# Kernel optimization log

Measured on AMD Instinct MI355X. Metric: run time of the kernel, lower is better.

Reference implementation:

```python
import jax, jax.numpy as jnp
import numpy as np

STRIDES = (8, 16, 32, 64, 128)
SCORE_THR = 0.05
IOU_THR = 0.6
MAX_NUM = 150
USE_CTR = True
B, NC = 64, 20
HW = (128, 64, 32, 16, 8)


def _reshape(feat):
    # [B,C,H,W] -> [B,H*W,C]
    b, c, h, w = feat.shape
    return feat.transpose(0, 2, 3, 1).reshape(b, h * w, c)


def _decode(feat, stride):
    # feat: [B,4,H,W] reg offsets; returns [B,HW,4] boxes (x1,y1,x2,y2)
    _, _, h, w = feat.shape
    xs = jnp.arange(w, dtype=jnp.float32) * stride + (stride // 2)
    ys = jnp.arange(h, dtype=jnp.float32) * stride + (stride // 2)
    yy, xx = jnp.meshgrid(ys, xs, indexing='ij')
    coords = jnp.stack([xx.reshape(-1), yy.reshape(-1)], axis=-1)  # [HW,2]
    off = _reshape(feat) * stride  # [B,HW,4]
    xy1 = coords[None] - off[..., :2]
    xy2 = coords[None] + off[..., 2:]
    return jnp.concatenate([xy1, xy2], axis=-1)


def _nms_single(scores, ids, boxes, valid):
    # scores already sorted descending (from top_k); class-aware offset NMS.
    coord_max = jnp.max(jnp.where(valid[:, None], boxes, -jnp.inf))
    coord_max = jnp.where(jnp.isfinite(coord_max), coord_max, 0.0)
    ob = boxes + (ids.astype(boxes.dtype) * (coord_max + 1.0))[:, None]
    x1, y1, x2, y2 = ob[:, 0], ob[:, 1], ob[:, 2], ob[:, 3]
    areas = (x2 - x1 + 1.0) * (y2 - y1 + 1.0)
    xmin = jnp.maximum(x1[:, None], x1[None, :])
    ymin = jnp.maximum(y1[:, None], y1[None, :])
    xmax = jnp.minimum(x2[:, None], x2[None, :])
    ymax = jnp.minimum(y2[:, None], y2[None, :])
    ow = jnp.clip(xmax - xmin, 0.0)
    oh = jnp.clip(ymax - ymin, 0.0)
    overlap = ow * oh
    union = jnp.clip(areas[:, None] + areas[None, :] - overlap, 1e-10)
    iou = overlap / union  # [N,N]
    n = scores.shape[0]
    idx = jnp.arange(n)

    def body(i, keep):
        sup = keep[i] & (iou[i] > IOU_THR) & (idx > i)
        return keep & ~sup

    return jax.lax.fori_loop(0, n, body, valid)


def setup_inputs() -> dict:
    key = jax.random.key(0)
    ks = jax.random.split(key, 15)
    out = {}
    for li, hw in enumerate(HW):
        out[f'cls{li}'] = jax.random.normal(ks[li], (B, NC, hw, hw), jnp.float32)
        out[f'reg{li}'] = jax.random.uniform(ks[5 + li], (B, 4, hw, hw), jnp.float32)
        out[f'ctr{li}'] = jax.random.normal(ks[10 + li], (B, 1, hw, hw), jnp.float32)
    return out


def reference(cls0, cls1, cls2, cls3, cls4,
              reg0, reg1, reg2, reg3, reg4,
              ctr0, ctr1, ctr2, ctr3, ctr4):
    cls_feats = (cls0, cls1, cls2, cls3, cls4)
    reg_feats = (reg0, reg1, reg2, reg3, reg4)
    ctr_feats = (ctr0, ctr1, ctr2, ctr3, ctr4)

    cls_logits = jnp.concatenate([_reshape(f) for f in cls_feats], axis=1)  # [B,A,NC]
    ctr_logits = jnp.concatenate([_reshape(f) for f in ctr_feats], axis=1)  # [B,A,1]
    cls_preds = jax.nn.sigmoid(cls_logits)
    ctr_preds = jax.nn.sigmoid(ctr_logits)

    cls_scores = jnp.max(cls_preds, axis=-1)  # [B,A]
    cls_ids = jnp.argmax(cls_preds, axis=-1) + 1  # [B,A]
    if USE_CTR:
        cls_scores = jnp.sqrt(cls_scores * ctr_preds[..., 0])

    boxes = jnp.concatenate(
        [_decode(f, s) for f, s in zip(reg_feats, STRIDES)], axis=1)  # [B,A,4]

    top_scores, top_idx = jax.lax.top_k(cls_scores, MAX_NUM)  # sorted desc
    top_ids = jnp.take_along_axis(cls_ids, top_idx, axis=1)
    top_boxes = jnp.take_along_axis(boxes, top_idx[..., None], axis=1)

    valid = top_scores > SCORE_THR
    keep = jax.vmap(_nms_single)(top_scores, top_ids, top_boxes, valid)

    out_scores = jnp.where(keep, top_scores, 0.0)
    out_ids = jnp.where(keep, top_ids, 0)
    out_boxes = jnp.where(keep[..., None], top_boxes, 0.0)
    return out_scores, out_ids, out_boxes, keep
```

## Files before the change

### kernel.cpp

```cpp
#include <hip/hip_runtime.h>
#include <cstdint>
#include <cstddef>

#define NPTS 21824
#define NB   64
#define NCLS 20
#define MAXN 150
#define NCHUNK 11
#define CHSZ 2048
#define CAP  186

typedef unsigned long long u64;
typedef unsigned int u32;


__device__ __forceinline__ u64 bisect_threshold(const u64 (&key)[8], int total,
                                                int (*wcnt)[4], int cap)
{
    const int tid  = threadIdx.x;
    const int lane = tid & 63, wv = tid >> 6;
    u64 T = 0;
    int count = total;
    int it = 0;
    for (int bbit = 62; bbit >= 0; --bbit) {
        if (bbit == 31) bbit = 14;
        if (count <= cap) break;
        u64 Tt = T | (1ull << bbit);
        int c = 0;
        #pragma unroll
        for (int i = 0; i < 8; ++i) c += (key[i] >= Tt) ? 1 : 0;
        for (int off = 32; off; off >>= 1) c += __shfl_xor(c, off);
        if (lane == 0) wcnt[it & 1][wv] = c;
        __syncthreads();
        int tot = wcnt[it & 1][0] + wcnt[it & 1][1]
                + wcnt[it & 1][2] + wcnt[it & 1][3];
        if (tot >= MAXN) { T = Tt; count = tot; }
        ++it;
    }
    return T;
}

__global__ __launch_bounds__(256) void k_part(
    const float* __restrict__ c0, const float* __restrict__ c1,
    const float* __restrict__ c2, const float* __restrict__ c3,
    const float* __restrict__ c4,
    const float* __restrict__ t0, const float* __restrict__ t1,
    const float* __restrict__ t2, const float* __restrict__ t3,
    const float* __restrict__ t4,
    u64* __restrict__ cand)
{
    __shared__ int wcnt[2][4];
    __shared__ int cnt;
    const int tid   = threadIdx.x;
    const int chunk = blockIdx.x;
    const int b     = blockIdx.y;
    const int pl    = tid * 8;
    const int p0    = chunk * CHSZ + pl;

    u64 key[8];
    #pragma unroll
    for (int i = 0; i < 8; ++i) key[i] = 0;

    if (p0 < NPTS) {
        const float* cp; const float* tp; int base; size_t hw;
        if (p0 < 16384)      { cp = c0; tp = t0; base = 0;     hw = 16384; }
        else if (p0 < 20480) { cp = c1; tp = t1; base = 16384; hw = 4096;  }
        else if (p0 < 21504) { cp = c2; tp = t2; base = 20480; hw = 1024;  }
        else if (p0 < 21760) { cp = c3; tp = t3; base = 21504; hw = 256;   }
        else                 { cp = c4; tp = t4; base = 21760; hw = 64;    }
        int q = p0 - base;
        const float* cb = cp + (size_t)b * NCLS * hw + q;

        float4 m0 = *reinterpret_cast<const float4*>(cb);
        float4 m1 = *reinterpret_cast<const float4*>(cb + 4);
        for (int c = 1; c < NCLS; ++c) {
            float4 v0 = *reinterpret_cast<const float4*>(cb + (size_t)c * hw);
            float4 v1 = *reinterpret_cast<const float4*>(cb + (size_t)c * hw + 4);
            m0.x = fmaxf(m0.x, v0.x); m0.y = fmaxf(m0.y, v0.y);
            m0.z = fmaxf(m0.z, v0.z); m0.w = fmaxf(m0.w, v0.w);
            m1.x = fmaxf(m1.x, v1.x); m1.y = fmaxf(m1.y, v1.y);
            m1.z = fmaxf(m1.z, v1.z); m1.w = fmaxf(m1.w, v1.w);
        }
        const float* tb = tp + (size_t)b * hw + q;
        float4 q0 = *reinterpret_cast<const float4*>(tb);
        float4 q1 = *reinterpret_cast<const float4*>(tb + 4);

        float mm[8] = {m0.x, m0.y, m0.z, m0.w, m1.x, m1.y, m1.z, m1.w};
        float cc[8] = {q0.x, q0.y, q0.z, q0.w, q1.x, q1.y, q1.z, q1.w};
        #pragma unroll
        for (int i = 0; i < 8; ++i) {
            float best = 1.0f / (1.0f + expf(-mm[i]));
            float sct  = 1.0f / (1.0f + expf(-cc[i]));
            float sc   = sqrtf(__fmul_rn(best, sct));
            key[i] = ((u64)__float_as_uint(sc) << 32)
                   | (u32)(21823 - (p0 + i));
        }
    }

    u64 T = bisect_threshold(key, CHSZ, wcnt, CAP);

    if (tid == 0) cnt = 0;
    __syncthreads();
    u64* outp = cand + ((size_t)b * NCHUNK + chunk) * CAP;
    #pragma unroll
    for (int i = 0; i < 8; ++i) {
        if (key[i] >= T) {
            int pos = atomicAdd(&cnt, 1);
            if (pos < CAP) outp[pos] = key[i];
        }
    }
    __syncthreads();
    for (int i = cnt + tid; i < CAP; i += 256) outp[i] = 0;
}

__global__ __launch_bounds__(256) void k_sel(
    const u64* __restrict__ cand, u64* __restrict__ srt_g)
{
    const int NC2 = NCHUNK * CAP;
    __shared__ int wcnt[2][4];
    __shared__ int cnt;
    __shared__ u64 win[CAP];

    const int b = blockIdx.x, tid = threadIdx.x;

    u64 key[8];
    #pragma unroll
    for (int j = 0; j < 8; ++j) {
        int i = j * 256 + tid;
        key[j] = (i < NC2) ? cand[(size_t)b * NC2 + i] : 0ull;
    }

    u64 T = bisect_threshold(key, CHSZ, wcnt, CAP);

    if (tid == 0) cnt = 0;
    __syncthreads();
    #pragma unroll
    for (int j = 0; j < 8; ++j) {
        if (key[j] >= T) {
            int pos = atomicAdd(&cnt, 1);
            if (pos < CAP) win[pos] = key[j];
        }
    }
    __syncthreads();
    int C = min(cnt, CAP);
    if (tid < C) {
        u64 mk = win[tid]; int r = 0;
        for (int j = 0; j < C; ++j) r += (win[j] > mk) ? 1 : 0;
        if (r < MAXN) srt_g[(size_t)b * MAXN + r] = mk;
    }
}

__global__ __launch_bounds__(1024) void k_out(
    const float* __restrict__ c0, const float* __restrict__ c1,
    const float* __restrict__ c2, const float* __restrict__ c3,
    const float* __restrict__ c4,
    const float* __restrict__ r0, const float* __restrict__ r1,
    const float* __restrict__ r2, const float* __restrict__ r3,
    const float* __restrict__ r4,
    const u64* __restrict__ srt_g,
    float* __restrict__ out)
{
    __shared__ int   parr[MAXN];
    __shared__ u64   pid[MAXN][4];
    __shared__ float bx0[MAXN], bx1[MAXN], bx2[MAXN], bx3[MAXN];
    __shared__ float ox1[MAXN], oy1[MAXN], ox2[MAXN], oy2[MAXN], area[MAXN];
    __shared__ float sc[MAXN];
    __shared__ int   idv[MAXN];
    __shared__ u64 sup[MAXN][3];
    __shared__ u64 keepw[3];
    __shared__ float shcmax;
    __shared__ float wmax[16];

    const int b = blockIdx.x, tid = threadIdx.x;

    if (tid < MAXN) {
        u64 kk = srt_g[(size_t)b * MAXN + tid];
        sc[tid]   = __uint_as_float((u32)(kk >> 32));
        parr[tid] = 21823 - (int)(kk & 0x7FFFu);
    }
    __syncthreads();

    if (tid < MAXN * 4) {
        int w = tid >> 2, g = tid & 3;
        int p = parr[w];
        const float* cp; int base; size_t hw;
        if (p < 16384)      { cp = c0; base = 0;     hw = 16384; }
        else if (p < 20480) { cp = c1; base = 16384; hw = 4096;  }
        else if (p < 21504) { cp = c2; base = 20480; hw = 1024;  }
        else if (p < 21760) { cp = c3; base = 21504; hw = 256;   }
        else                { cp = c4; base = 21760; hw = 64;    }
        const float* cb = cp + (size_t)b * NCLS * hw + (p - base);
        float best = -1.0f; int bi = 0;
        #pragma unroll
        for (int j = 0; j < 5; ++j) {
            int c = g * 5 + j;
            float v  = cb[(size_t)c * hw];
            float sg = 1.0f / (1.0f + expf(-v));
            if (sg > best) { best = sg; bi = c; }
        }
        pid[w][g] = ((u64)__float_as_uint(best) << 32) | (u32)(31 - bi);
    } else if (tid < MAXN * 4 + MAXN) {
        int w = tid - MAXN * 4;
        int p = parr[w];
        const float* rp; int base, dim, lg, st;
        if (p < 16384)      { rp = r0; base = 0;     dim = 128; lg = 7; st = 8;   }
        else if (p < 20480) { rp = r1; base = 16384; dim = 64;  lg = 6; st = 16;  }
        else if (p < 21504) { rp = r2; base = 20480; dim = 32;  lg = 5; st = 32;  }
        else if (p < 21760) { rp = r3; base = 21504; dim = 16;  lg = 4; st = 64;  }
        else                { rp = r4; base = 21760; dim = 8;   lg = 3; st = 128; }
        int q = p - base;
        int y = q >> lg;
        int x = q & (dim - 1);
        float s  = (float)st;
        float cx = (float)(x * st + (st >> 1));
        float cy = (float)(y * st + (st >> 1));
        size_t hw = (size_t)dim * dim;
        const float* rg = rp + (size_t)b * 4 * hw + q;
        float a0 = rg[0], a1 = rg[hw], a2 = rg[2 * hw], a3 = rg[3 * hw];
        bx0[w] = __fsub_rn(cx, __fmul_rn(a0, s));
        bx1[w] = __fsub_rn(cy, __fmul_rn(a1, s));
        bx2[w] = __fadd_rn(cx, __fmul_rn(a2, s));
        bx3[w] = __fadd_rn(cy, __fmul_rn(a3, s));
    }
    __syncthreads();

    if (tid < MAXN) {
        u64 m0 = pid[tid][0], m1 = pid[tid][1];
        u64 m2 = pid[tid][2], m3 = pid[tid][3];
        u64 mbest = m0;
        if (m1 > mbest) mbest = m1;
        if (m2 > mbest) mbest = m2;
        if (m3 > mbest) mbest = m3;
        idv[tid] = (31 - (int)(mbest & 31u)) + 1;
    }
    __syncthreads();

    float m = -INFINITY;
    if (tid < MAXN && sc[tid] > 0.05f)
        m = fmaxf(fmaxf(bx0[tid], bx1[tid]), fmaxf(bx2[tid], bx3[tid]));
    #pragma unroll
    for (int off = 32; off >= 1; off >>= 1) m = fmaxf(m, __shfl_xor(m, off));
    if ((tid & 63) == 0) wmax[tid >> 6] = m;
    if (tid < 192) {
        bool val = (tid < MAXN) && (sc[tid] > 0.05f);
        u64 mask = __ballot(val);
        if ((tid & 63) == 0) keepw[tid >> 6] = mask;
    }
    __syncthreads();
    if (tid == 0) {
        float mm = -INFINITY;
        #pragma unroll
        for (int w = 0; w < 16; ++w) mm = fmaxf(mm, wmax[w]);
        shcmax = isfinite(mm) ? mm : 0.0f;
    }
    __syncthreads();

    float cm1 = __fadd_rn(shcmax, 1.0f);
    if (tid < MAXN) {
        float off = __fmul_rn((float)idv[tid], cm1);
        float X1 = __fadd_rn(bx0[tid], off);
        float Y1 = __fadd_rn(bx1[tid], off);
        float X2 = __fadd_rn(bx2[tid], off);
        float Y2 = __fadd_rn(bx3[tid], off);
        ox1[tid] = X1; oy1[tid] = Y1; ox2[tid] = X2; oy2[tid] = Y2;
        area[tid] = __fmul_rn(__fadd_rn(__fsub_rn(X2, X1), 1.0f),
                              __fadd_rn(__fsub_rn(Y2, Y1), 1.0f));
    }
    __syncthreads();

    if (tid < MAXN * 3) {
        int i = tid / 3;
        int w = tid - i * 3;
        float x1i = ox1[i], y1i = oy1[i], x2i = ox2[i], y2i = oy2[i], ai = area[i];
        u64 bits = 0ull;
        for (int e = 0; e < 64; ++e) {
            int j = w * 64 + e;
            if (j >= MAXN) break;
            float xmin = fmaxf(x1i, ox1[j]);
            float ymin = fmaxf(y1i, oy1[j]);
            float xmax = fminf(x2i, ox2[j]);
            float ymax = fminf(y2i, oy2[j]);
            float ow = fmaxf(__fsub_rn(xmax, xmin), 0.0f);
            float oh = fmaxf(__fsub_rn(ymax, ymin), 0.0f);
            float ov = __fmul_rn(ow, oh);
            float un = fmaxf(__fsub_rn(__fadd_rn(ai, area[j]), ov), 1e-10f);
            float iou = __fdiv_rn(ov, un);
            if (iou > 0.6f) bits |= (1ull << e);
        }
        sup[i][w] = bits;
    }
    __syncthreads();

    if (tid < 64) {
        const int l = tid;
        u64 kw   = (l < 3) ? keepw[l]  : 0ull;
        u64 scur = (l < 3) ? sup[0][l] : 0ull;
        for (int i = 0; i < MAXN; ++i) {
            u64 snext = (l < 3 && i + 1 < MAXN) ? sup[i + 1][l] : 0ull;
            u64 kwwi = __shfl(kw, i >> 6);
            if ((kwwi >> (i & 63)) & 1ull) {
                int lo = l * 64;
                u64 allow;
                if (i < lo)            allow = ~0ull;
                else if (i - lo >= 63) allow = 0ull;
                else                   allow = ~((1ull << (i - lo + 1)) - 1ull);
                kw &= ~(scur & allow);
            }
            scur = snext;
        }
        if (l < 3) keepw[l] = kw;
    }
    __syncthreads();

    if (tid < MAXN) {
        bool kp = (keepw[tid >> 6] >> (tid & 63)) & 1ull;
        int o = b * MAXN + tid;
        float* oSc = out;
        float* oId = out + NB * MAXN;
        float* oBx = out + 2 * NB * MAXN;
        float* oKp = out + 2 * NB * MAXN + NB * MAXN * 4;
        oSc[o] = kp ? sc[tid] : 0.0f;
        oId[o] = kp ? (float)idv[tid] : 0.0f;
        oBx[o * 4 + 0] = kp ? bx0[tid] : 0.0f;
        oBx[o * 4 + 1] = kp ? bx1[tid] : 0.0f;
        oBx[o * 4 + 2] = kp ? bx2[tid] : 0.0f;
        oBx[o * 4 + 3] = kp ? bx3[tid] : 0.0f;
        oKp[o] = kp ? 1.0f : 0.0f;
    }
}

extern "C" void kernel_launch(void* const* d_in, const int* in_sizes, int n_in,
                              void* d_out, int out_size, void* d_ws, size_t ws_size,
                              hipStream_t stream)
{
    const float* cls[5]; const float* reg[5]; const float* ctr[5];
    for (int li = 0; li < 5; ++li) {
        cls[li] = (const float*)d_in[3 * li + 0];
        reg[li] = (const float*)d_in[3 * li + 1];
        ctr[li] = (const float*)d_in[3 * li + 2];
    }

    const size_t CAND_BYTES = (size_t)NB * NCHUNK * CAP * sizeof(u64);
    u64* cand  = (u64*)d_ws;
    u64* srt_g = (u64*)((char*)d_ws + CAND_BYTES);

    dim3 g1(NCHUNK, NB);
    k_part<<<g1, 256, 0, stream>>>(cls[0], cls[1], cls[2], cls[3], cls[4],
                                   ctr[0], ctr[1], ctr[2], ctr[3], ctr[4],
                                   cand);
    k_sel<<<NB, 256, 0, stream>>>(cand, srt_g);
    k_out<<<NB, 1024, 0, stream>>>(cls[0], cls[1], cls[2], cls[3], cls[4],
                                   reg[0], reg[1], reg[2], reg[3], reg[4],
                                   srt_g, (float*)d_out);
}
```

Before: 246.7 us.

## Fuse candidate selection into output kernel and widen partition blocks to 512 threads

The separate selection kernel is folded into the output/NMS kernel, so the top-150 window is kept in shared memory instead of going through global memory and an extra launch. The partition kernel now uses 512 threads handling 4 points each instead of 256 threads handling 8, giving more independent loads in flight. The bisection helper is templated on block size and keys per thread. In exchange, the output kernel runs with 512 threads and loops over its gather work, and it now carries the serial selection step at the start of each block.

```diff
diff --git a/kernel.cpp b/kernel.cpp
--- a/kernel.cpp
+++ b/kernel.cpp
@@ -14,11 +14,14 @@
 typedef unsigned int u32;
 
 
-__device__ __forceinline__ u64 bisect_threshold(const u64 (&key)[8], int total,
-                                                int (*wcnt)[4], int cap)
+template<int TPB, int K>
+__device__ __forceinline__ u64 bisect_threshold(const u64 (&key)[K],
+                                                int (*wcnt)[TPB / 64],
+                                                int total, int cap)
 {
     const int tid  = threadIdx.x;
     const int lane = tid & 63, wv = tid >> 6;
+    constexpr int NW = TPB / 64;
     u64 T = 0;
     int count = total;
     int it = 0;
@@ -28,19 +31,21 @@
         u64 Tt = T | (1ull << bbit);
         int c = 0;
         #pragma unroll
-        for (int i = 0; i < 8; ++i) c += (key[i] >= Tt) ? 1 : 0;
+        for (int i = 0; i < K; ++i) c += (key[i] >= Tt) ? 1 : 0;
+        #pragma unroll
         for (int off = 32; off; off >>= 1) c += __shfl_xor(c, off);
         if (lane == 0) wcnt[it & 1][wv] = c;
         __syncthreads();
-        int tot = wcnt[it & 1][0] + wcnt[it & 1][1]
-                + wcnt[it & 1][2] + wcnt[it & 1][3];
+        int tot = 0;
+        #pragma unroll
+        for (int w = 0; w < NW; ++w) tot += wcnt[it & 1][w];
         if (tot >= MAXN) { T = Tt; count = tot; }
         ++it;
     }
     return T;
 }
 
-__global__ __launch_bounds__(256) void k_part(
+__global__ __launch_bounds__(512, 4) void k_part(
     const float* __restrict__ c0, const float* __restrict__ c1,
     const float* __restrict__ c2, const float* __restrict__ c3,
     const float* __restrict__ c4,
@@ -49,17 +54,14 @@
     const float* __restrict__ t4,
     u64* __restrict__ cand)
 {
-    __shared__ int wcnt[2][4];
+    __shared__ int wcnt[2][8];
     __shared__ int cnt;
     const int tid   = threadIdx.x;
     const int chunk = blockIdx.x;
     const int b     = blockIdx.y;
-    const int pl    = tid * 8;
-    const int p0    = chunk * CHSZ + pl;
-
-    u64 key[8];
-    #pragma unroll
-    for (int i = 0; i < 8; ++i) key[i] = 0;
+    const int p0    = chunk * CHSZ + tid * 4;
+
+    u64 key[4] = {0ull, 0ull, 0ull, 0ull};
 
     if (p0 < NPTS) {
         const float* cp; const float* tp; int base; size_t hw;
@@ -71,95 +73,58 @@
         int q = p0 - base;
         const float* cb = cp + (size_t)b * NCLS * hw + q;
 
-        float4 m0 = *reinterpret_cast<const float4*>(cb);
-        float4 m1 = *reinterpret_cast<const float4*>(cb + 4);
+        float4 mx = *reinterpret_cast<const float4*>(cb);
+        #pragma unroll
         for (int c = 1; c < NCLS; ++c) {
-            float4 v0 = *reinterpret_cast<const float4*>(cb + (size_t)c * hw);
-            float4 v1 = *reinterpret_cast<const float4*>(cb + (size_t)c * hw + 4);
-            m0.x = fmaxf(m0.x, v0.x); m0.y = fmaxf(m0.y, v0.y);
-            m0.z = fmaxf(m0.z, v0.z); m0.w = fmaxf(m0.w, v0.w);
-            m1.x = fmaxf(m1.x, v1.x); m1.y = fmaxf(m1.y, v1.y);
-            m1.z = fmaxf(m1.z, v1.z); m1.w = fmaxf(m1.w, v1.w);
-        }
-        const float* tb = tp + (size_t)b * hw + q;
-        float4 q0 = *reinterpret_cast<const float4*>(tb);
-        float4 q1 = *reinterpret_cast<const float4*>(tb + 4);
-
-        float mm[8] = {m0.x, m0.y, m0.z, m0.w, m1.x, m1.y, m1.z, m1.w};
-        float cc[8] = {q0.x, q0.y, q0.z, q0.w, q1.x, q1.y, q1.z, q1.w};
-        #pragma unroll
-        for (int i = 0; i < 8; ++i) {
+            float4 v = *reinterpret_cast<const float4*>(cb + (size_t)c * hw);
+            mx.x = fmaxf(mx.x, v.x); mx.y = fmaxf(mx.y, v.y);
+            mx.z = fmaxf(mx.z, v.z); mx.w = fmaxf(mx.w, v.w);
+        }
+        float4 cv = *reinterpret_cast<const float4*>(tp + (size_t)b * hw + q);
+
+        float mm[4] = {mx.x, mx.y, mx.z, mx.w};
+        float cc[4] = {cv.x, cv.y, cv.z, cv.w};
+        #pragma unroll
+        for (int i = 0; i < 4; ++i) {
             float best = 1.0f / (1.0f + expf(-mm[i]));
             float sct  = 1.0f / (1.0f + expf(-cc[i]));
-            float sc   = sqrtf(__fmul_rn(best, sct));
-            key[i] = ((u64)__float_as_uint(sc) << 32)
+            float s    = sqrtf(__fmul_rn(best, sct));
+            key[i] = ((u64)__float_as_uint(s) << 32)
                    | (u32)(21823 - (p0 + i));
         }
     }
 
-    u64 T = bisect_threshold(key, CHSZ, wcnt, CAP);
+    u64 T = bisect_threshold<512, 4>(key, wcnt, CHSZ, CAP);
 
     if (tid == 0) cnt = 0;
     __syncthreads();
     u64* outp = cand + ((size_t)b * NCHUNK + chunk) * CAP;
     #pragma unroll
-    for (int i = 0; i < 8; ++i) {
+    for (int i = 0; i < 4; ++i) {
         if (key[i] >= T) {
             int pos = atomicAdd(&cnt, 1);
             if (pos < CAP) outp[pos] = key[i];
         }
     }
     __syncthreads();
-    for (int i = cnt + tid; i < CAP; i += 256) outp[i] = 0;
+    for (int i = cnt + tid; i < CAP; i += 512) outp[i] = 0;
 }
 
-__global__ __launch_bounds__(256) void k_sel(
-    const u64* __restrict__ cand, u64* __restrict__ srt_g)
-{
-    const int NC2 = NCHUNK * CAP;
-    __shared__ int wcnt[2][4];
-    __shared__ int cnt;
-    __shared__ u64 win[CAP];
-
-    const int b = blockIdx.x, tid = threadIdx.x;
-
-    u64 key[8];
-    #pragma unroll
-    for (int j = 0; j < 8; ++j) {
-        int i = j * 256 + tid;
-        key[j] = (i < NC2) ? cand[(size_t)b * NC2 + i] : 0ull;
-    }
-
-    u64 T = bisect_threshold(key, CHSZ, wcnt, CAP);
-
-    if (tid == 0) cnt = 0;
-    __syncthreads();
-    #pragma unroll
-    for (int j = 0; j < 8; ++j) {
-        if (key[j] >= T) {
-            int pos = atomicAdd(&cnt, 1);
-            if (pos < CAP) win[pos] = key[j];
-        }
-    }
-    __syncthreads();
-    int C = min(cnt, CAP);
-    if (tid < C) {
-        u64 mk = win[tid]; int r = 0;
-        for (int j = 0; j < C; ++j) r += (win[j] > mk) ? 1 : 0;
-        if (r < MAXN) srt_g[(size_t)b * MAXN + r] = mk;
-    }
-}
-
-__global__ __launch_bounds__(1024) void k_out(
+__global__ __launch_bounds__(512) void k_out(
     const float* __restrict__ c0, const float* __restrict__ c1,
     const float* __restrict__ c2, const float* __restrict__ c3,
     const float* __restrict__ c4,
     const float* __restrict__ r0, const float* __restrict__ r1,
     const float* __restrict__ r2, const float* __restrict__ r3,
     const float* __restrict__ r4,
-    const u64* __restrict__ srt_g,
+    const u64* __restrict__ cand,
     float* __restrict__ out)
 {
+    const int NC2 = NCHUNK * CAP;
+    __shared__ int wcnt[2][8];
+    __shared__ int cnt;
+    __shared__ u64 win[CAP];
+    __shared__ u64 srt[MAXN];
     __shared__ int   parr[MAXN];
     __shared__ u64   pid[MAXN][4];
     __shared__ float bx0[MAXN], bx1[MAXN], bx2[MAXN], bx3[MAXN];
@@ -169,58 +134,88 @@
     __shared__ u64 sup[MAXN][3];
     __shared__ u64 keepw[3];
     __shared__ float shcmax;
-    __shared__ float wmax[16];
+    __shared__ float wmax[8];
 
     const int b = blockIdx.x, tid = threadIdx.x;
 
+    u64 key[4];
+    #pragma unroll
+    for (int j = 0; j < 4; ++j) {
+        int i = j * 512 + tid;
+        key[j] = (i < NC2) ? cand[(size_t)b * NC2 + i] : 0ull;
+    }
+
+    u64 T = bisect_threshold<512, 4>(key, wcnt, 2048, CAP);
+
+    if (tid == 0) cnt = 0;
+    if (tid < MAXN) srt[tid] = 0ull;
+    __syncthreads();
+    #pragma unroll
+    for (int j = 0; j < 4; ++j) {
+        if (key[j] >= T) {
+            int pos = atomicAdd(&cnt, 1);
+            if (pos < CAP) win[pos] = key[j];
+        }
+    }
+    __syncthreads();
+    int C = min(cnt, CAP);
+    if (tid < C) {
+        u64 mk = win[tid]; int r = 0;
+        for (int j = 0; j < C; ++j) r += (win[j] > mk) ? 1 : 0;
+        if (r < MAXN) srt[r] = mk;
+    }
+    __syncthreads();
+
     if (tid < MAXN) {
-        u64 kk = srt_g[(size_t)b * MAXN + tid];
+        u64 kk = srt[tid];
         sc[tid]   = __uint_as_float((u32)(kk >> 32));
         parr[tid] = 21823 - (int)(kk & 0x7FFFu);
     }
     __syncthreads();
 
-    if (tid < MAXN * 4) {
-        int w = tid >> 2, g = tid & 3;
-        int p = parr[w];
-        const float* cp; int base; size_t hw;
-        if (p < 16384)      { cp = c0; base = 0;     hw = 16384; }
-        else if (p < 20480) { cp = c1; base = 16384; hw = 4096;  }
-        else if (p < 21504) { cp = c2; base = 20480; hw = 1024;  }
-        else if (p < 21760) { cp = c3; base = 21504; hw = 256;   }
-        else                { cp = c4; base = 21760; hw = 64;    }
-        const float* cb = cp + (size_t)b * NCLS * hw + (p - base);
-        float best = -1.0f; int bi = 0;
-        #pragma unroll
-        for (int j = 0; j < 5; ++j) {
-            int c = g * 5 + j;
-            float v  = cb[(size_t)c * hw];
-            float sg = 1.0f / (1.0f + expf(-v));
-            if (sg > best) { best = sg; bi = c; }
-        }
-        pid[w][g] = ((u64)__float_as_uint(best) << 32) | (u32)(31 - bi);
-    } else if (tid < MAXN * 4 + MAXN) {
-        int w = tid - MAXN * 4;
-        int p = parr[w];
-        const float* rp; int base, dim, lg, st;
-        if (p < 16384)      { rp = r0; base = 0;     dim = 128; lg = 7; st = 8;   }
-        else if (p < 20480) { rp = r1; base = 16384; dim = 64;  lg = 6; st = 16;  }
-        else if (p < 21504) { rp = r2; base = 20480; dim = 32;  lg = 5; st = 32;  }
-        else if (p < 21760) { rp = r3; base = 21504; dim = 16;  lg = 4; st = 64;  }
-        else                { rp = r4; base = 21760; dim = 8;   lg = 3; st = 128; }
-        int q = p - base;
-        int y = q >> lg;
-        int x = q & (dim - 1);
-        float s  = (float)st;
-        float cx = (float)(x * st + (st >> 1));
-        float cy = (float)(y * st + (st >> 1));
-        size_t hw = (size_t)dim * dim;
-        const float* rg = rp + (size_t)b * 4 * hw + q;
-        float a0 = rg[0], a1 = rg[hw], a2 = rg[2 * hw], a3 = rg[3 * hw];
-        bx0[w] = __fsub_rn(cx, __fmul_rn(a0, s));
-        bx1[w] = __fsub_rn(cy, __fmul_rn(a1, s));
-        bx2[w] = __fadd_rn(cx, __fmul_rn(a2, s));
-        bx3[w] = __fadd_rn(cy, __fmul_rn(a3, s));
+    for (int t = tid; t < MAXN * 5; t += 512) {
+        if (t < MAXN * 4) {
+            int w = t >> 2, g = t & 3;
+            int p = parr[w];
+            const float* cp; int base; size_t hw;
+            if (p < 16384)      { cp = c0; base = 0;     hw = 16384; }
+            else if (p < 20480) { cp = c1; base = 16384; hw = 4096;  }
+            else if (p < 21504) { cp = c2; base = 20480; hw = 1024;  }
+            else if (p < 21760) { cp = c3; base = 21504; hw = 256;   }
+            else                { cp = c4; base = 21760; hw = 64;    }
+            const float* cb = cp + (size_t)b * NCLS * hw + (p - base);
+            float best = -1.0f; int bi = 0;
+            #pragma unroll
+            for (int j = 0; j < 5; ++j) {
+                int c = g * 5 + j;
+                float v  = cb[(size_t)c * hw];
+                float sg = 1.0f / (1.0f + expf(-v));
+                if (sg > best) { best = sg; bi = c; }
+            }
+            pid[w][g] = ((u64)__float_as_uint(best) << 32) | (u32)(31 - bi);
+        } else {
+            int w = t - MAXN * 4;
+            int p = parr[w];
+            const float* rp; int base, dim, lg, st;
+            if (p < 16384)      { rp = r0; base = 0;     dim = 128; lg = 7; st = 8;   }
+            else if (p < 20480) { rp = r1; base = 16384; dim = 64;  lg = 6; st = 16;  }
+            else if (p < 21504) { rp = r2; base = 20480; dim = 32;  lg = 5; st = 32;  }
+            else if (p < 21760) { rp = r3; base = 21504; dim = 16;  lg = 4; st = 64;  }
+            else                { rp = r4; base = 21760; dim = 8;   lg = 3; st = 128; }
+            int q = p - base;
+            int y = q >> lg;
+            int x = q & (dim - 1);
+            float s  = (float)st;
+            float cx = (float)(x * st + (st >> 1));
+            float cy = (float)(y * st + (st >> 1));
+            size_t hw = (size_t)dim * dim;
+            const float* rg = rp + (size_t)b * 4 * hw + q;
+            float a0 = rg[0], a1 = rg[hw], a2 = rg[2 * hw], a3 = rg[3 * hw];
+            bx0[w] = __fsub_rn(cx, __fmul_rn(a0, s));
+            bx1[w] = __fsub_rn(cy, __fmul_rn(a1, s));
+            bx2[w] = __fadd_rn(cx, __fmul_rn(a2, s));
+            bx3[w] = __fadd_rn(cy, __fmul_rn(a3, s));
+        }
     }
     __syncthreads();
 
@@ -250,7 +245,7 @@
     if (tid == 0) {
         float mm = -INFINITY;
         #pragma unroll
-        for (int w = 0; w < 16; ++w) mm = fmaxf(mm, wmax[w]);
+        for (int w = 0; w < 8; ++w) mm = fmaxf(mm, wmax[w]);
         shcmax = isfinite(mm) ? mm : 0.0f;
     }
     __syncthreads();
@@ -340,16 +335,13 @@
         ctr[li] = (const float*)d_in[3 * li + 2];
     }
 
-    const size_t CAND_BYTES = (size_t)NB * NCHUNK * CAP * sizeof(u64);
-    u64* cand  = (u64*)d_ws;
-    u64* srt_g = (u64*)((char*)d_ws + CAND_BYTES);
+    u64* cand = (u64*)d_ws;
 
     dim3 g1(NCHUNK, NB);
-    k_part<<<g1, 256, 0, stream>>>(cls[0], cls[1], cls[2], cls[3], cls[4],
+    k_part<<<g1, 512, 0, stream>>>(cls[0], cls[1], cls[2], cls[3], cls[4],
                                    ctr[0], ctr[1], ctr[2], ctr[3], ctr[4],
                                    cand);
-    k_sel<<<NB, 256, 0, stream>>>(cand, srt_g);
-    k_out<<<NB, 1024, 0, stream>>>(cls[0], cls[1], cls[2], cls[3], cls[4],
-                                   reg[0], reg[1], reg[2], reg[3], reg[4],
-                                   srt_g, (float*)d_out);
+    k_out<<<NB, 512, 0, stream>>>(cls[0], cls[1], cls[2], cls[3], cls[4],
+                                  reg[0], reg[1], reg[2], reg[3], reg[4],
+                                  cand, (float*)d_out);
 }
```

Measured after the change: 238.1 us. 3.5% less time.
